# Optimization experiments

Hardware: AMD Instinct MI355X
Metric: run time of the kernel (lower is better)

Reference implementation:

```python
import jax, jax.numpy as jnp
import numpy as np

A, B, S, D = 4, 8, 2048, 256   # agents, batch, seq_len, encode_dim
L = 3                          # layer_num


def setup_inputs() -> dict:
    key = jax.random.key(0)
    ks = jax.random.split(key, 13)
    sD = 1.0 / np.sqrt(D)
    s2D = 1.0 / np.sqrt(2 * D)
    return {
        'x':   jax.random.normal(ks[0], (A, B, S, D), jnp.float32),
        'W3':  jax.random.normal(ks[1], (D, D), jnp.float32) * sD,
        'b3':  jnp.zeros((D,), jnp.float32),
        'W4':  jax.random.normal(ks[2], (D, D), jnp.float32) * sD,
        'b4':  jnp.zeros((D,), jnp.float32),
        'Wx_f': jax.random.normal(ks[3], (D, 4 * D), jnp.float32) * sD,
        'Wh_f': jax.random.normal(ks[4], (D, 4 * D), jnp.float32) * sD,
        'b_f':  jnp.zeros((4 * D,), jnp.float32),
        'Wx_b': jax.random.normal(ks[5], (D, 4 * D), jnp.float32) * sD,
        'Wh_b': jax.random.normal(ks[6], (D, 4 * D), jnp.float32) * sD,
        'b_b':  jnp.zeros((4 * D,), jnp.float32),
        'Wd':  jax.random.normal(ks[7], (2 * D, D), jnp.float32) * s2D,
        'bd':  jnp.zeros((D,), jnp.float32),
    }


def _lstm(x, Wx, Wh, b):
    # x: [N, S, D] -> hidden sequence [N, S, H]; standard (CuDNN) LSTM, gates i,f,c,o
    H = Wh.shape[0]
    xw = jnp.einsum('nsd,dh->nsh', x, Wx) + b          # precompute input projections

    def step(carry, xt):
        h, c = carry
        g = xt + h @ Wh                                 # [N, 4H]
        i, f, g2, o = jnp.split(g, 4, axis=-1)
        i = jax.nn.sigmoid(i)
        f = jax.nn.sigmoid(f)
        g2 = jnp.tanh(g2)
        o = jax.nn.sigmoid(o)
        c = f * c + i * g2
        h = o * jnp.tanh(c)
        return (h, c), h

    N = x.shape[0]
    init = (jnp.zeros((N, H), x.dtype), jnp.zeros((N, H), x.dtype))
    _, hs = jax.lax.scan(step, init, jnp.swapaxes(xw, 0, 1))  # scan over time
    return jnp.swapaxes(hs, 0, 1)


def _bilstm(x, Wx_f, Wh_f, b_f, Wx_b, Wh_b, b_b):
    fwd = _lstm(x, Wx_f, Wh_f, b_f)
    bwd = _lstm(x[:, ::-1], Wx_b, Wh_b, b_b)[:, ::-1]
    return jnp.concatenate([fwd, bwd], axis=-1)        # merge_mode='concat'


def reference(x, W3, b3, W4, b4, Wx_f, Wh_f, b_f, Wx_b, Wh_b, b_b, Wd, bd):
    # x: [A, B, S, D] stacked agent local-encoder outputs
    h = x
    for _ in range(L - 1):
        # z: sum of last-timestep states over ALL agents, divided by (A-1) (faithful quirk)
        z = h[:, :, -1, :].sum(axis=0) / (A - 1)       # [B, D]
        zp = (z @ W4 + b4)[None, :, None, :]           # broadcast over agents & time
        f = jnp.tanh(jnp.einsum('absd,de->abse', h, W3) + b3 + zp)  # [A,B,S,D]
        y = _bilstm(f.reshape(A * B, S, D), Wx_f, Wh_f, b_f, Wx_b, Wh_b, b_b)  # [A*B,S,2D]
        h = (y @ Wd + bd).reshape(A, B, S, D)
    return h
```

## Files before the change

kernel.cpp:

```cpp
#include <hip/hip_runtime.h>
#include <hip/hip_bf16.h>

#define SEQ 2048
#define DH  256

typedef unsigned short ushort_t;
typedef __attribute__((ext_vector_type(8))) _Float16 half8;
typedef __attribute__((ext_vector_type(4))) _Float16 half4;
typedef __attribute__((ext_vector_type(8))) short   short8;
typedef __attribute__((ext_vector_type(4))) float   floatx4;

static __device__ __forceinline__ float bf2f(ushort_t u){
    union { unsigned int i; float f; } v; v.i = ((unsigned int)u) << 16; return v.f;
}
static __device__ __forceinline__ ushort_t f2bf(float f){
    union { float f; unsigned int i; } v; v.f = f;
    unsigned int r = v.i + 0x7fff + ((v.i >> 16) & 1);
    return (ushort_t)(r >> 16);
}
static __device__ __forceinline__ float fsig(float x){
    return __builtin_amdgcn_rcpf(1.f + __expf(-x));
}
static __device__ __forceinline__ float ftanh(float x){
    float e = __expf(-2.f * fabsf(x));
    float r = (1.f - e) * __builtin_amdgcn_rcpf(1.f + e);
    return copysignf(r, x);
}

__global__ void detect_kernel(const ushort_t* __restrict__ x, unsigned int* flag){
    __shared__ int cnt[256];
    int c = 0;
    for (int i = threadIdx.x; i < 4096; i += 256) {
        int e = (x[i] >> 7) & 0xFF;
        c += (e >= 0x60 && e <= 0x9F);
    }
    cnt[threadIdx.x] = c;
    __syncthreads();
    for (int s = 128; s > 0; s >>= 1) {
        if (threadIdx.x < s) cnt[threadIdx.x] += cnt[threadIdx.x + s];
        __syncthreads();
    }
    if (threadIdx.x == 0) *flag = (cnt[0] >= 3686) ? 0u : 1u;
}

__global__ void convert_kernel(const void* __restrict__ src, ushort_t* __restrict__ dst,
                               int n, const unsigned int* __restrict__ flag){
    int i = blockIdx.x * 256 + threadIdx.x;
    if (i >= n) return;
    if (*flag) dst[i] = f2bf(((const float*)src)[i]);
    else       dst[i] = ((const ushort_t*)src)[i];
}

__global__ void tohalf_kernel(const ushort_t* __restrict__ src, _Float16* __restrict__ dst, int n){
    int i = blockIdx.x * 256 + threadIdx.x;
    if (i < n) dst[i] = (_Float16)bf2f(src[i]);
}

__global__ void zp_kernel(const void* __restrict__ hin,
                          const ushort_t* __restrict__ W4,
                          const ushort_t* __restrict__ b4,
                          float* __restrict__ zp,
                          const unsigned int* __restrict__ flag, int dyn)
{
    __shared__ float zl[8 * 256];
    const int isf32 = dyn ? (int)*flag : 0;
    const int tid = threadIdx.x;
    for (int i = tid; i < 8 * 256; i += 256) {
        int b = i >> 8, d = i & 255;
        float s = 0.f;
        #pragma unroll
        for (int a = 0; a < 4; ++a) {
            size_t idx = (((size_t)(a * 8 + b)) * SEQ + (SEQ - 1)) * DH + d;
            s += isf32 ? ((const float*)hin)[idx] : bf2f(((const ushort_t*)hin)[idx]);
        }
        zl[i] = s * (1.f / 3.f);
    }
    __syncthreads();
    float acc[8] = {0,0,0,0,0,0,0,0};
    for (int k = 0; k < 256; ++k) {
        float w = bf2f(W4[k * 256 + tid]);
        #pragma unroll
        for (int b = 0; b < 8; ++b) acc[b] += zl[b * 256 + k] * w;
    }
    float bias = bf2f(b4[tid]);
    #pragma unroll
    for (int b = 0; b < 8; ++b) zp[b * 256 + tid] = acc[b] + bias;
}

__global__ void zero_out_kernel(ushort_t* o, int n){
    int i = blockIdx.x * 256 + threadIdx.x;
    if (i < n) o[i] = 0;
}

__global__ void wtrans_kernel(const ushort_t* __restrict__ Whf,
                              const ushort_t* __restrict__ Whb,
                              _Float16* __restrict__ Wp)
{
    const int fb = blockIdx.x;
    const int kt = fb & 7, g = (fb >> 3) & 3, cc = (fb >> 5) & 15, dir = fb >> 9;
    const int lane = threadIdx.x;
    const ushort_t* Wh = dir ? Whb : Whf;
    _Float16 v[8];
    #pragma unroll
    for (int j = 0; j < 8; ++j)
        v[j] = (_Float16)bf2f(Wh[(size_t)(kt * 32 + (lane >> 4) * 8 + j) * 1024
                                 + g * 256 + cc * 16 + (lane & 15)]);
    *(half8*)(Wp + ((size_t)fb * 64 + lane) * 8) = *(const half8*)v;
}

template<int MODE, int KTILES, bool OUT_HALF, int CHLOG, bool DYNA, bool OUT_DYN, bool TMAJ,
         int AMODE = 0, bool F16 = false>
__global__ __launch_bounds__(256)
void gemm_kernel(const void* __restrict__ A0,
                 const ushort_t* __restrict__ A1,
                 const ushort_t* __restrict__ Bmat,
                 const ushort_t* __restrict__ bias,
                 const float*    __restrict__ zp,
                 void* __restrict__ Cout, int N, int t0,
                 const unsigned int* __restrict__ flag)
{
    __shared__ ushort_t As[128 * 32];
    __shared__ ushort_t Bt[64 * 40];

    const int tid  = threadIdx.x;
    const int lane = tid & 63, wid = tid >> 6;
    const int quad = lane >> 4, l16 = lane & 15;
    const int col0 = blockIdx.x * 64;
    const int row0 = blockIdx.y * 128;
    const int isf32 = (DYNA || OUT_DYN) ? (int)*flag : 0;

    floatx4 acc[2][4] = {};

    #pragma unroll
    for (int kb = 0; kb < KTILES; ++kb) {
        const void* Asrc = A0;
        int kA = kb * 32;
        if (MODE == 2 && kb >= 8) { Asrc = (const void*)A1; kA = (kb - 8) * 32; }
        const int kB = kb * 32;

        const int ar = tid >> 2, asg = tid & 3;
        const int r1 = row0 + ar, r2 = r1 + 64;
        size_t ar1, ar2;
        if constexpr (AMODE == 2) {
            ar1 = (size_t)(r1 & 31) * SEQ + t0 + (r1 >> 5);
            ar2 = (size_t)(r2 & 31) * SEQ + t0 + (r2 >> 5);
        } else if constexpr (AMODE == 3) {
            ar1 = (size_t)(r1 & (SEQ - 1)) * 32 + (r1 >> 11);
            ar2 = (size_t)(r2 & (SEQ - 1)) * 32 + (r2 >> 11);
        } else if (CHLOG) {
            ar1 = ((size_t)(r1 >> CHLOG)) * SEQ + t0 + (r1 & ((1 << CHLOG) - 1));
            ar2 = ((size_t)(r2 >> CHLOG)) * SEQ + t0 + (r2 & ((1 << CHLOG) - 1));
        } else { ar1 = (size_t)r1; ar2 = (size_t)r2; }
        const size_t e1 = ar1 * 256 + kA + asg * 8;
        const size_t e2 = ar2 * 256 + kA + asg * 8;
        uint4 av0, av1;
        if (DYNA && isf32) {
            const float* f1 = (const float*)Asrc + e1;
            const float* f2 = (const float*)Asrc + e2;
            float4 a = *(const float4*)f1, b = *(const float4*)(f1 + 4);
            float4 c = *(const float4*)f2, d = *(const float4*)(f2 + 4);
            ushort_t u0[8] = {f2bf(a.x),f2bf(a.y),f2bf(a.z),f2bf(a.w),
                              f2bf(b.x),f2bf(b.y),f2bf(b.z),f2bf(b.w)};
            ushort_t u1[8] = {f2bf(c.x),f2bf(c.y),f2bf(c.z),f2bf(c.w),
                              f2bf(d.x),f2bf(d.y),f2bf(d.z),f2bf(d.w)};
            av0 = *(const uint4*)u0; av1 = *(const uint4*)u1;
        } else {
            av0 = *(const uint4*)((const ushort_t*)Asrc + e1);
            av1 = *(const uint4*)((const ushort_t*)Asrc + e2);
        }

        const int bn = tid & 63, bkr = tid >> 6;
        ushort_t bv[8];
        #pragma unroll
        for (int p = 0; p < 8; ++p)
            bv[p] = Bmat[(size_t)(kB + bkr * 8 + p) * N + col0 + bn];

        __syncthreads();
        *(uint4*)&As[ar * 32 + asg * 8]        = av0;
        *(uint4*)&As[(ar + 64) * 32 + asg * 8] = av1;
        #pragma unroll
        for (int p = 0; p < 8; ++p)
            Bt[bn * 40 + bkr * 8 + p] = bv[p];
        __syncthreads();

        short8 af[2], bfr[4];
        af[0] = *(const short8*)&As[(wid * 32 +      l16) * 32 + quad * 8];
        af[1] = *(const short8*)&As[(wid * 32 + 16 + l16) * 32 + quad * 8];
        #pragma unroll
        for (int ct = 0; ct < 4; ++ct)
            bfr[ct] = *(const short8*)&Bt[(ct * 16 + l16) * 40 + quad * 8];
        #pragma unroll
        for (int rt = 0; rt < 2; ++rt)
            #pragma unroll
            for (int ct = 0; ct < 4; ++ct) {
                if constexpr (F16)
                    acc[rt][ct] = __builtin_amdgcn_mfma_f32_16x16x32_f16(
                        *(const half8*)&af[rt], *(const half8*)&bfr[ct], acc[rt][ct], 0, 0, 0);
                else
                    acc[rt][ct] = __builtin_amdgcn_mfma_f32_16x16x32_bf16(
                        af[rt], bfr[ct], acc[rt][ct], 0, 0, 0);
            }
    }

    if constexpr (AMODE == 2) {
        const int tt = (row0 + wid * 32) >> 5;
        #pragma unroll
        for (int ct = 0; ct < 4; ++ct) {
            const int n = col0 + ct * 16 + l16;
            const float bz = bf2f(bias[n]);
            #pragma unroll
            for (int rt = 0; rt < 2; ++rt) {
                _Float16 v4[4];
                #pragma unroll
                for (int r = 0; r < 4; ++r)
                    v4[r] = (_Float16)(acc[rt][ct][r] + bz);
                *(half4*)((_Float16*)Cout + ((size_t)tt * N + n) * 32 + rt * 16 + quad * 4)
                    = *(const half4*)v4;
            }
        }
    } else {
        #pragma unroll
        for (int ct = 0; ct < 4; ++ct) {
            const int n = col0 + ct * 16 + l16;
            const float bz = bf2f(bias[n]);
            #pragma unroll
            for (int rt = 0; rt < 2; ++rt) {
                #pragma unroll
                for (int r = 0; r < 4; ++r) {
                    const int row = row0 + wid * 32 + rt * 16 + quad * 4 + r;
                    size_t orow = (size_t)row;
                    if (TMAJ) orow = (size_t)(row & ((1 << CHLOG) - 1)) * 32 + (row >> CHLOG);
                    float v = acc[rt][ct][r] + bz;
                    if (MODE == 1) v = ftanh(v + zp[((row >> 11) & 7) * N + n]);
                    if (OUT_HALF)
                        ((_Float16*)Cout)[orow * N + n] = (_Float16)v;
                    else if (OUT_DYN && isf32)
                        ((float*)Cout)[orow * N + n] = v;
                    else
                        ((ushort_t*)Cout)[orow * N + n] = f2bf(v);
                }
            }
        }
    }
}

__global__ __launch_bounds__(128, 1)
void lstm_kernel(const _Float16* __restrict__ xwf, const _Float16* __restrict__ xwb,
                 const _Float16* __restrict__ Wp,
                 _Float16* __restrict__ hsf, _Float16* __restrict__ hsb,
                 unsigned int* flags, float* cstate,
                 int s0, int clen)
{
    const int xcd = blockIdx.x & 7, q = blockIdx.x >> 3;
    if (xcd >= 2) return;
    const int dir = xcd;

    const int tid = threadIdx.x, lane = tid & 63, w = tid >> 6;
    const int quad = lane >> 4, l16 = lane & 15;
    const int ccl = w;
    const int col = q * 32 + ccl * 16 + l16;

    const _Float16* xw = dir ? xwb : xwf;
    _Float16* hs = dir ? hsb : hsf;
    unsigned int* fl = flags + dir * 512;
    unsigned int* myflag = fl + q * 64;
    float* cs = cstate + dir * 8192;

    __shared__ __align__(16) _Float16 wlds[32768];
    {
        const char* src = (const char*)(Wp + (size_t)(dir * 16 + q * 2) * 32 * 512);
        #pragma unroll
        for (int i = 0; i < 32; ++i) {
            const int idx = i * 128 + tid;
            *(uint4*)((char*)wlds + (size_t)idx * 16) =
                *(const uint4*)(src + (size_t)idx * 16);
        }
    }
    __syncthreads();

    float creg[2][4];
    #pragma unroll
    for (int mt = 0; mt < 2; ++mt)
        #pragma unroll
        for (int r = 0; r < 4; ++r)
            creg[mt][r] = s0 ? cs[(mt * 16 + quad * 4 + r) * 256 + col] : 0.f;

    uint2 xcur[2][4], xnxt[2][4];
    auto load_x = [&](uint2 (*dst)[4], int ssn) {
        int tr2 = dir ? (clen - 1 - ssn) : ssn;
        tr2 = tr2 < 0 ? 0 : (tr2 > clen - 1 ? clen - 1 : tr2);
        #pragma unroll
        for (int mt = 0; mt < 2; ++mt)
            #pragma unroll
            for (int g = 0; g < 4; ++g)
                dst[mt][g] = *(const uint2*)(xw + ((size_t)tr2 * 1024 + g * 256 + col) * 32
                                             + mt * 16 + quad * 4);
    };
    load_x(xcur, 0);

    for (int ss = 0; ss < clen; ++ss) {
        const int s = s0 + ss;
        const int t = dir ? (SEQ - 1 - s) : s;

        half8 af[2][8];
        if (s > 0) {
            if (lane < 8) {
                const unsigned int tgt = (unsigned int)s;
                int guard = 0;
                while (__hip_atomic_load(fl + lane * 64, __ATOMIC_RELAXED,
                                         __HIP_MEMORY_SCOPE_AGENT) < tgt)
                    if (++guard > (1 << 22)) break;
            }
            asm volatile("" ::: "memory");
            const int tp = dir ? (t + 1) : (t - 1);
            #pragma unroll
            for (int mt = 0; mt < 2; ++mt)
                #pragma unroll
                for (int kt = 0; kt < 8; ++kt) {
                    const unsigned long long* p = (const unsigned long long*)
                        (hs + ((size_t)tp * 32 + mt * 16 + l16) * 256 + kt * 32 + quad * 8);
                    unsigned long long lo = __hip_atomic_load(p,     __ATOMIC_RELAXED, __HIP_MEMORY_SCOPE_AGENT);
                    unsigned long long hi = __hip_atomic_load(p + 1, __ATOMIC_RELAXED, __HIP_MEMORY_SCOPE_AGENT);
                    union { unsigned long long u[2]; half8 v; } uu;
                    uu.u[0] = lo; uu.u[1] = hi;
                    af[mt][kt] = uu.v;
                }
        } else {
            #pragma unroll
            for (int mt = 0; mt < 2; ++mt)
                #pragma unroll
                for (int kt = 0; kt < 8; ++kt)
                    af[mt][kt] = half8{};
        }

        floatx4 acc[2][4] = {};
        #pragma unroll
        for (int kt = 0; kt < 8; ++kt)
            #pragma unroll
            for (int g = 0; g < 4; ++g) {
                const half8 bf = *(const half8*)&wlds[(size_t)(ccl * 32 + g * 8 + kt) * 512
                                                      + lane * 8];
                acc[0][g] = __builtin_amdgcn_mfma_f32_16x16x32_f16(af[0][kt], bf, acc[0][g], 0, 0, 0);
                acc[1][g] = __builtin_amdgcn_mfma_f32_16x16x32_f16(af[1][kt], bf, acc[1][g], 0, 0, 0);
            }

        #pragma unroll
        for (int mt = 0; mt < 2; ++mt)
            #pragma unroll
            for (int r = 0; r < 4; ++r) {
                const int row = mt * 16 + quad * 4 + r;
                float gi = fsig (acc[mt][0][r] + (float)((const _Float16*)&xcur[mt][0])[r]);
                float gf = fsig (acc[mt][1][r] + (float)((const _Float16*)&xcur[mt][1])[r]);
                float gg = ftanh(acc[mt][2][r] + (float)((const _Float16*)&xcur[mt][2])[r]);
                float go = fsig (acc[mt][3][r] + (float)((const _Float16*)&xcur[mt][3])[r]);
                float c = gf * creg[mt][r] + gi * gg;
                creg[mt][r] = c;
                float h = go * ftanh(c);
                union { _Float16 h; ushort_t u; } cv; cv.h = (_Float16)h;
                __hip_atomic_store((ushort_t*)(hs + ((size_t)t * 32 + row) * 256 + col),
                                   cv.u, __ATOMIC_RELAXED, __HIP_MEMORY_SCOPE_AGENT);
            }

        asm volatile("" ::: "memory");
        load_x(xnxt, ss + 1);
        asm volatile("s_waitcnt vmcnt(8)" ::: "memory");
        __builtin_amdgcn_s_barrier();
        if (tid == 0)
            __hip_atomic_store(myflag, (unsigned int)(s + 1),
                               __ATOMIC_RELAXED, __HIP_MEMORY_SCOPE_AGENT);

        #pragma unroll
        for (int mt = 0; mt < 2; ++mt)
            #pragma unroll
            for (int g = 0; g < 4; ++g) xcur[mt][g] = xnxt[mt][g];
    }

    #pragma unroll
    for (int mt = 0; mt < 2; ++mt)
        #pragma unroll
        for (int r = 0; r < 4; ++r)
            cs[(mt * 16 + quad * 4 + r) * 256 + col] = creg[mt][r];
}

extern "C" void kernel_launch(void* const* d_in, const int* in_sizes, int n_in,
                              void* d_out, int out_size, void* d_ws, size_t ws_size,
                              hipStream_t stream)
{
    const void* x = d_in[0];

    const size_t MB = 1048576;
    int chlog;
    if      (ws_size >= 165 * MB) chlog = 9;
    else if (ws_size >= 133 * MB) chlog = 8;
    else {
        zero_out_kernel<<<(out_size + 255) / 256, 256, 0, stream>>>(
            (ushort_t*)d_out, out_size);
        return;
    }
    const int clen = 1 << chlog;
    const int nch  = SEQ >> chlog;
    const size_t xwsz = (size_t)32 * clen * 1024 * sizeof(_Float16);

    char* ws = (char*)d_ws;
    unsigned int* flags0 = (unsigned int*)ws;
    unsigned int* flag = (unsigned int*)(ws + 8192);
    float*    zp     = (float*)(ws + 12288);
    float*    cstate = (float*)(ws + 20480);
    ushort_t* WC     = (ushort_t*)(ws + 262144);
    ushort_t* F    = (ushort_t*)(ws + 3   * MB);
    _Float16* Wp   = (_Float16*)(ws + 35  * MB);
    _Float16* HSF  = (_Float16*)(ws + 36  * MB);
    _Float16* HSB  = (_Float16*)(ws + 68  * MB);
    _Float16* XWFc = (_Float16*)(ws + 100 * MB);
    _Float16* XWBc = (_Float16*)(ws + 100 * MB + xwsz);
    ushort_t* HN   = (ushort_t*)(ws + 100 * MB);
    _Float16* Wdh  = (_Float16*)(ws + 100 * MB + 2 * xwsz);

    ushort_t* W3c  = WC;
    ushort_t* b3c  = WC + 65536;
    ushort_t* W4c  = WC + 65792;
    ushort_t* b4c  = WC + 131328;
    ushort_t* Wxfc = WC + 131584;
    ushort_t* Whfc = WC + 393728;
    ushort_t* bfc  = WC + 655872;
    ushort_t* Wxbc = WC + 656896;
    ushort_t* Whbc = WC + 919040;
    ushort_t* bbc  = WC + 1181184;
    ushort_t* Wdc  = WC + 1182208;
    ushort_t* bdc  = WC + 1313280;

    hipMemsetAsync(ws, 0, 8192, stream);

    detect_kernel<<<1, 256, 0, stream>>>((const ushort_t*)x, flag);

    ushort_t* dsts[12] = {W3c,b3c,W4c,b4c,Wxfc,Whfc,bfc,Wxbc,Whbc,bbc,Wdc,bdc};
    const int  cnts[12] = {65536,256,65536,256,262144,262144,1024,
                           262144,262144,1024,131072,256};
    for (int i = 0; i < 12; ++i)
        convert_kernel<<<(cnts[i] + 255) / 256, 256, 0, stream>>>(
            d_in[i + 1], dsts[i], cnts[i], flag);

    tohalf_kernel<<<512, 256, 0, stream>>>(Wdc, Wdh, 131072);
    wtrans_kernel<<<1024, 64, 0, stream>>>(Whfc, Whbc, Wp);

    for (int l = 0; l < 2; ++l) {
        const void* hin = (l == 0) ? x : (const void*)HN;
        void* hout = (l == 1) ? d_out : (void*)HN;

        zp_kernel<<<1, 256, 0, stream>>>(hin, W4c, b4c, zp, flag, l == 0 ? 1 : 0);
        if (l == 0)
            gemm_kernel<1, 8, false, 0, true, false, false><<<dim3(4, 512), 256, 0, stream>>>(
                hin, nullptr, W3c, b3c, zp, F, 256, 0, flag);
        else
            gemm_kernel<1, 8, false, 0, false, false, false><<<dim3(4, 512), 256, 0, stream>>>(
                hin, nullptr, W3c, b3c, zp, F, 256, 0, flag);

        const int gy = 32 * clen / 128;
        for (int c = 0; c < nch; ++c) {
            const int t0f = c * clen;
            const int t0b = SEQ - (c + 1) * clen;
            gemm_kernel<0, 8, true, 0, false, false, false, 2, false><<<dim3(16, gy), 256, 0, stream>>>(
                F, nullptr, Wxfc, bfc, nullptr, XWFc, 1024, t0f, flag);
            gemm_kernel<0, 8, true, 0, false, false, false, 2, false><<<dim3(16, gy), 256, 0, stream>>>(
                F, nullptr, Wxbc, bbc, nullptr, XWBc, 1024, t0b, flag);
            lstm_kernel<<<64, 128, 0, stream>>>(
                XWFc, XWBc, Wp, HSF, HSB,
                flags0 + l * 1024, cstate, c * clen, clen);
        }

        if (l == 1)
            gemm_kernel<2, 16, false, 0, false, true, false, 3, true><<<dim3(4, 512), 256, 0, stream>>>(
                (const void*)HSF, (const ushort_t*)HSB, (const ushort_t*)Wdh, bdc,
                nullptr, hout, 256, 0, flag);
        else
            gemm_kernel<2, 16, false, 0, false, false, false, 3, true><<<dim3(4, 512), 256, 0, stream>>>(
                (const void*)HSF, (const ushort_t*)HSB, (const ushort_t*)Wdh, bdc,
                nullptr, hout, 256, 0, flag);
    }
}
```

Baseline: 16.27 ms.

## Replace LSTM per-step flag barrier with sentinel-poisoned hidden-state polling

Removes the per-step flag counters, the workgroup barrier and the flag store between cooperating LSTM blocks. Instead, each hidden-state buffer is filled with 0xFFFF (a NaN fp16 pattern) before each layer, and consumers spin re-reading the previous step's h values until no 16-bit lane equals the sentinel. The next-step x prefetch also moves earlier. This cuts the serial step's synchronisation latency but adds two large memsets per layer and depends on a real h never encoding as 0xFFFF and on the 16-bit stores being seen atomically.

```diff
diff --git a/kernel.cpp b/kernel.cpp
--- a/kernel.cpp
+++ b/kernel.cpp
@@ -25,6 +25,9 @@
     float e = __expf(-2.f * fabsf(x));
     float r = (1.f - e) * __builtin_amdgcn_rcpf(1.f + e);
     return copysignf(r, x);
+}
+static __device__ __forceinline__ unsigned long long chkFFFF(unsigned long long x){
+    return ((~x) - 0x0001000100010001ull) & x & 0x8000800080008000ull;
 }
 
 __global__ void detect_kernel(const ushort_t* __restrict__ x, unsigned int* flag){
@@ -248,8 +251,7 @@
 void lstm_kernel(const _Float16* __restrict__ xwf, const _Float16* __restrict__ xwb,
                  const _Float16* __restrict__ Wp,
                  _Float16* __restrict__ hsf, _Float16* __restrict__ hsb,
-                 unsigned int* flags, float* cstate,
-                 int s0, int clen)
+                 float* cstate, int s0, int clen)
 {
     const int xcd = blockIdx.x & 7, q = blockIdx.x >> 3;
     if (xcd >= 2) return;
@@ -262,8 +264,6 @@
 
     const _Float16* xw = dir ? xwb : xwf;
     _Float16* hs = dir ? hsb : hsf;
-    unsigned int* fl = flags + dir * 512;
-    unsigned int* myflag = fl + q * 64;
     float* cs = cstate + dir * 8192;
 
     __shared__ __align__(16) _Float16 wlds[32768];
@@ -298,33 +298,33 @@
     };
     load_x(xcur, 0);
 
+    int gb = 1 << 17;
+
     for (int ss = 0; ss < clen; ++ss) {
         const int s = s0 + ss;
         const int t = dir ? (SEQ - 1 - s) : s;
 
         half8 af[2][8];
         if (s > 0) {
-            if (lane < 8) {
-                const unsigned int tgt = (unsigned int)s;
-                int guard = 0;
-                while (__hip_atomic_load(fl + lane * 64, __ATOMIC_RELAXED,
-                                         __HIP_MEMORY_SCOPE_AGENT) < tgt)
-                    if (++guard > (1 << 22)) break;
-            }
-            asm volatile("" ::: "memory");
             const int tp = dir ? (t + 1) : (t - 1);
-            #pragma unroll
-            for (int mt = 0; mt < 2; ++mt)
+            const _Float16* hb = hs + (size_t)tp * 8192;
+            unsigned long long bad;
+            do {
+                bad = 0;
                 #pragma unroll
-                for (int kt = 0; kt < 8; ++kt) {
-                    const unsigned long long* p = (const unsigned long long*)
-                        (hs + ((size_t)tp * 32 + mt * 16 + l16) * 256 + kt * 32 + quad * 8);
-                    unsigned long long lo = __hip_atomic_load(p,     __ATOMIC_RELAXED, __HIP_MEMORY_SCOPE_AGENT);
-                    unsigned long long hi = __hip_atomic_load(p + 1, __ATOMIC_RELAXED, __HIP_MEMORY_SCOPE_AGENT);
-                    union { unsigned long long u[2]; half8 v; } uu;
-                    uu.u[0] = lo; uu.u[1] = hi;
-                    af[mt][kt] = uu.v;
-                }
+                for (int mt = 0; mt < 2; ++mt)
+                    #pragma unroll
+                    for (int kt = 0; kt < 8; ++kt) {
+                        const unsigned long long* p = (const unsigned long long*)
+                            (hb + (mt * 16 + l16) * 256 + kt * 32 + quad * 8);
+                        unsigned long long lo = __hip_atomic_load(p,     __ATOMIC_RELAXED, __HIP_MEMORY_SCOPE_AGENT);
+                        unsigned long long hi = __hip_atomic_load(p + 1, __ATOMIC_RELAXED, __HIP_MEMORY_SCOPE_AGENT);
+                        bad |= chkFFFF(lo) | chkFFFF(hi);
+                        union { unsigned long long u[2]; half8 v; } uu;
+                        uu.u[0] = lo; uu.u[1] = hi;
+                        af[mt][kt] = uu.v;
+                    }
+            } while (bad != 0 && --gb > 0);
         } else {
             #pragma unroll
             for (int mt = 0; mt < 2; ++mt)
@@ -332,6 +332,8 @@
                 for (int kt = 0; kt < 8; ++kt)
                     af[mt][kt] = half8{};
         }
+
+        load_x(xnxt, ss + 1);
 
         floatx4 acc[2][4] = {};
         #pragma unroll
@@ -361,14 +363,6 @@
                                    cv.u, __ATOMIC_RELAXED, __HIP_MEMORY_SCOPE_AGENT);
             }
 
-        asm volatile("" ::: "memory");
-        load_x(xnxt, ss + 1);
-        asm volatile("s_waitcnt vmcnt(8)" ::: "memory");
-        __builtin_amdgcn_s_barrier();
-        if (tid == 0)
-            __hip_atomic_store(myflag, (unsigned int)(s + 1),
-                               __ATOMIC_RELAXED, __HIP_MEMORY_SCOPE_AGENT);
-
         #pragma unroll
         for (int mt = 0; mt < 2; ++mt)
             #pragma unroll
@@ -400,9 +394,9 @@
     const int clen = 1 << chlog;
     const int nch  = SEQ >> chlog;
     const size_t xwsz = (size_t)32 * clen * 1024 * sizeof(_Float16);
+    const size_t hssz = (size_t)SEQ * 32 * 256 * sizeof(_Float16);
 
     char* ws = (char*)d_ws;
-    unsigned int* flags0 = (unsigned int*)ws;
     unsigned int* flag = (unsigned int*)(ws + 8192);
     float*    zp     = (float*)(ws + 12288);
     float*    cstate = (float*)(ws + 20480);
@@ -429,8 +423,6 @@
     ushort_t* Wdc  = WC + 1182208;
     ushort_t* bdc  = WC + 1313280;
 
-    hipMemsetAsync(ws, 0, 8192, stream);
-
     detect_kernel<<<1, 256, 0, stream>>>((const ushort_t*)x, flag);
 
     ushort_t* dsts[12] = {W3c,b3c,W4c,b4c,Wxfc,Whfc,bfc,Wxbc,Whbc,bbc,Wdc,bdc};
@@ -446,6 +438,9 @@
     for (int l = 0; l < 2; ++l) {
         const void* hin = (l == 0) ? x : (const void*)HN;
         void* hout = (l == 1) ? d_out : (void*)HN;
+
+        hipMemsetAsync(HSF, 0xFF, hssz, stream);
+        hipMemsetAsync(HSB, 0xFF, hssz, stream);
 
         zp_kernel<<<1, 256, 0, stream>>>(hin, W4c, b4c, zp, flag, l == 0 ? 1 : 0);
         if (l == 0)
@@ -464,8 +459,7 @@
             gemm_kernel<0, 8, true, 0, false, false, false, 2, false><<<dim3(16, gy), 256, 0, stream>>>(
                 F, nullptr, Wxbc, bbc, nullptr, XWBc, 1024, t0b, flag);
             lstm_kernel<<<64, 128, 0, stream>>>(
-                XWFc, XWBc, Wp, HSF, HSB,
-                flags0 + l * 1024, cstate, c * clen, clen);
+                XWFc, XWBc, Wp, HSF, HSB, cstate, c * clen, clen);
         }
 
         if (l == 1)
```

Result: slower. 21.72 ms (+33.5%).
